# Performance work log

Hardware: AMD Instinct MI355X
Metric: run time of the kernel (lower is better)

Reference implementation:

```python
import jax, jax.numpy as jnp
import numpy as np

N, D_OUT, D_LAT, D_Z = 65536, 128, 64, 64


def setup_inputs() -> dict:
    key = jax.random.key(0)
    ks = jax.random.split(key, 6)
    return {
        "target": jax.random.normal(ks[0], (N, D_OUT), dtype=jnp.float32),
        "output": jax.random.normal(ks[1], (N, D_OUT), dtype=jnp.float32),
        "mean": jax.random.normal(ks[2], (N, D_LAT), dtype=jnp.float32),
        "log_variance": jax.random.normal(ks[3], (N, D_LAT), dtype=jnp.float32),
        "z_t": jax.random.normal(ks[4], (N, D_Z), dtype=jnp.float32),
        "z_t_tau": jax.random.normal(ks[5], (N, D_Z), dtype=jnp.float32),
    }


def reference(target, output, mean, log_variance, z_t, z_t_tau):
    # ELBO: KL(q||N(0,1)) per-sample summed over latent dim, then batch mean
    kl = -0.5 * jnp.sum(log_variance - jnp.exp(log_variance) - mean ** 2 + 1.0, axis=1)
    kl = jnp.mean(kl)
    # reconstruction MSE (weights=None path)
    reconstruction = jnp.mean((output - target) ** 2)
    elbo_loss = reconstruction + kl

    # autocorrelation: diagonal of z_t_centered @ z_t_tau_centered.T is just
    # a rowwise dot product -> O(N*D) instead of O(N^2*D)
    z_t_centered = z_t - jnp.mean(z_t, axis=0)          # [N, D_z]
    z_t_tau_centered = z_t_tau - jnp.mean(z_t_tau, axis=0)
    diag = jnp.sum(z_t_centered * z_t_tau_centered, axis=1)  # [N]
    auto_correlation_loss = -jnp.mean(diag)

    # torch .std() is unbiased (ddof=1)
    std_t = jnp.std(z_t, axis=0, ddof=1)                # [D_z]
    std_tau = jnp.std(z_t_tau, axis=0, ddof=1)
    auto_correlation_loss = auto_correlation_loss / jnp.dot(std_t, std_tau)

    return elbo_loss + auto_correlation_loss
```

## Files before the change

### kernel.cpp

```cpp
#include <hip/hip_runtime.h>

constexpr int N_ROWS  = 65536;
constexpr int THREADS = 256;
constexpr int B_MSE = 1024, B_KL = 512, B_Z = 512;
constexpr int BLOCKS = B_MSE + B_KL + B_Z;
constexpr int F4_BLK = 2048;
constexpr int IT     = F4_BLK / THREADS;

constexpr int NVAL = 324;
constexpr int NREP = 64;

typedef float f4v __attribute__((ext_vector_type(4)));

__device__ __forceinline__ f4v ntload(const f4v* p) {
    return __builtin_nontemporal_load(p);
}


__global__ __launch_bounds__(THREADS) void vde_main(
    const f4v* __restrict__ target,
    const f4v* __restrict__ output,
    const f4v* __restrict__ mean,
    const f4v* __restrict__ logvar,
    const f4v* __restrict__ zt,
    const f4v* __restrict__ ztau,
    float* __restrict__ ws)
{
    const int lane = threadIdx.x & 63;
    const int wave = threadIdx.x >> 6;
    float* rep = ws + (blockIdx.x & (NREP - 1)) * NVAL;

    __shared__ float ssc[4];
    __shared__ float sred[4][16][20];

    if (blockIdx.x < B_MSE) {
        const int base = blockIdx.x * F4_BLK + threadIdx.x;
        float recon = 0.f;
        #pragma unroll
        for (int it = 0; it < IT; ++it) {
            f4v o = ntload(&output[base + it * THREADS]);
            f4v t = ntload(&target[base + it * THREADS]);
            f4v d = o - t;
            recon += d[0]*d[0] + d[1]*d[1] + d[2]*d[2] + d[3]*d[3];
        }
        #pragma unroll
        for (int m = 32; m >= 1; m >>= 1) recon += __shfl_xor(recon, m);
        if (lane == 0) ssc[wave] = recon;
        __syncthreads();
        if (threadIdx.x == 0)
            atomicAdd(&rep[0], ssc[0] + ssc[1] + ssc[2] + ssc[3]);

    } else if (blockIdx.x < B_MSE + B_KL) {
        const int base = (blockIdx.x - B_MSE) * F4_BLK + threadIdx.x;
        float kls = 0.f;
        #pragma unroll
        for (int it = 0; it < IT; ++it) {
            f4v lv = ntload(&logvar[base + it * THREADS]);
            f4v m  = ntload(&mean[base + it * THREADS]);
            kls += (lv[0] - __expf(lv[0]) - m[0]*m[0] + 1.f)
                 + (lv[1] - __expf(lv[1]) - m[1]*m[1] + 1.f)
                 + (lv[2] - __expf(lv[2]) - m[2]*m[2] + 1.f)
                 + (lv[3] - __expf(lv[3]) - m[3]*m[3] + 1.f);
        }
        #pragma unroll
        for (int m = 32; m >= 1; m >>= 1) kls += __shfl_xor(kls, m);
        if (lane == 0) ssc[wave] = kls;
        __syncthreads();
        if (threadIdx.x == 0)
            atomicAdd(&rep[1], ssc[0] + ssc[1] + ssc[2] + ssc[3]);

    } else {
        const int base = (blockIdx.x - B_MSE - B_KL) * F4_BLK + threadIdx.x;
        float s_t[4] = {0,0,0,0}, s_t2[4] = {0,0,0,0};
        float s_a[4] = {0,0,0,0}, s_a2[4] = {0,0,0,0}, s_c[4] = {0,0,0,0};
        #pragma unroll
        for (int it = 0; it < IT; ++it) {
            f4v a = ntload(&zt[base + it * THREADS]);
            f4v b = ntload(&ztau[base + it * THREADS]);
            #pragma unroll
            for (int e = 0; e < 4; ++e) {
                s_t[e]  += a[e];       s_a[e]  += b[e];
                s_t2[e] += a[e]*a[e];  s_a2[e] += b[e]*b[e];
                s_c[e]  += a[e]*b[e];
            }
        }
        float vals[20];
        #pragma unroll
        for (int e = 0; e < 4; ++e) {
            vals[e*5+0] = s_t[e];  vals[e*5+1] = s_a[e];
            vals[e*5+2] = s_t2[e]; vals[e*5+3] = s_a2[e];
            vals[e*5+4] = s_c[e];
        }
        #pragma unroll
        for (int v = 0; v < 20; ++v) {
            vals[v] += __shfl_xor(vals[v], 16);
            vals[v] += __shfl_xor(vals[v], 32);
        }
        if (lane < 16) {
            #pragma unroll
            for (int v = 0; v < 20; ++v) sred[wave][lane][v] = vals[v];
        }
        __syncthreads();
        for (int i = threadIdx.x; i < 320; i += THREADS) {
            const int g = i / 20, v = i % 20;
            const float s = sred[0][g][v] + sred[1][g][v]
                          + sred[2][g][v] + sred[3][g][v];
            const int e = v / 5, st = v % 5;
            atomicAdd(&rep[2 + st * 64 + (g * 4 + e)], s);
        }
    }
}

__global__ __launch_bounds__(256) void vde_tail(
    const float* __restrict__ ws, float* __restrict__ out)
{
    __shared__ float sums[NVAL];
    for (int j = threadIdx.x; j < NVAL; j += 256) {
        float s = 0.f;
        #pragma unroll
        for (int r = 0; r < NREP; ++r) s += ws[r * NVAL + j];
        sums[j] = s;
    }
    __syncthreads();

    if (threadIdx.x < 64) {
        const int j = threadIdx.x;
        const float Nf = (float)N_ROWS;
        const float sum_t  = sums[2 + 0*64 + j];
        const float sum_a  = sums[2 + 1*64 + j];
        const float sum_t2 = sums[2 + 2*64 + j];
        const float sum_a2 = sums[2 + 3*64 + j];
        const float sum_c  = sums[2 + 4*64 + j];

        const float mu_t = sum_t / Nf, mu_a = sum_a / Nf;
        float diag = sum_c - Nf * mu_t * mu_a;
        const float var_t = (sum_t2 - Nf * mu_t * mu_t) / (Nf - 1.f);
        const float var_a = (sum_a2 - Nf * mu_a * mu_a) / (Nf - 1.f);
        float sp = sqrtf(var_t) * sqrtf(var_a);

        #pragma unroll
        for (int m = 32; m >= 1; m >>= 1) {
            diag += __shfl_xor(diag, m);
            sp   += __shfl_xor(sp, m);
        }
        if (j == 0) {
            const float recon_f = sums[0] / (Nf * 128.f);
            const float kl_f    = -0.5f * sums[1] / Nf;
            out[0] = recon_f + kl_f - (diag / Nf) / sp;
        }
    }
}

extern "C" void kernel_launch(void* const* d_in, const int* in_sizes, int n_in,
                              void* d_out, int out_size, void* d_ws, size_t ws_size,
                              hipStream_t stream) {
    const f4v* target = (const f4v*)d_in[0];
    const f4v* output = (const f4v*)d_in[1];
    const f4v* mean   = (const f4v*)d_in[2];
    const f4v* logvar = (const f4v*)d_in[3];
    const f4v* zt     = (const f4v*)d_in[4];
    const f4v* ztau   = (const f4v*)d_in[5];
    float* ws  = (float*)d_ws;
    float* out = (float*)d_out;

    hipMemsetAsync(ws, 0, NREP * NVAL * sizeof(float), stream);
    vde_main<<<BLOCKS, THREADS, 0, stream>>>(target, output, mean, logvar, zt, ztau, ws);
    vde_tail<<<1, 256, 0, stream>>>(ws, out);
}
```

Measured before the change: 148.0 us.

## Fuse tail reduction into main kernel via last-block ticket and per-block partials

Removes the separate tail kernel: each block increments a ticket counter, and the last block to finish does the final reduction and writes the loss. The MSE and KL partials are now plain stores into per-block slots instead of atomics into contended replicas. All loads are issued up front into register arrays to raise memory-level parallelism. This saves one kernel launch and its gap, at the cost of more registers and a serial final reduction inside the last block.

```diff
diff --git a/kernel.cpp b/kernel.cpp
--- a/kernel.cpp
+++ b/kernel.cpp
@@ -7,40 +7,52 @@
 constexpr int F4_BLK = 2048;
 constexpr int IT     = F4_BLK / THREADS;
 
-constexpr int NVAL = 324;
-constexpr int NREP = 64;
+constexpr int NREP  = 64;
+constexpr int NZVAL = 320;
+constexpr int TICKET  = NREP * NZVAL;
+constexpr int MSE_OFF = TICKET + 1;
+constexpr int KL_OFF  = MSE_OFF + B_MSE;
+constexpr int MEMSET_BYTES = (TICKET + 1) * 4;
 
 typedef float f4v __attribute__((ext_vector_type(4)));
 
 __device__ __forceinline__ f4v ntload(const f4v* p) {
     return __builtin_nontemporal_load(p);
 }
-
-
-__global__ __launch_bounds__(THREADS) void vde_main(
+__device__ __forceinline__ float agent_load(const float* p) {
+    return __hip_atomic_load(p, __ATOMIC_RELAXED, __HIP_MEMORY_SCOPE_AGENT);
+}
+__device__ __forceinline__ void agent_store(float* p, float v) {
+    __hip_atomic_store(p, v, __ATOMIC_RELAXED, __HIP_MEMORY_SCOPE_AGENT);
+}
+
+__global__ __launch_bounds__(THREADS) void vde_fused(
     const f4v* __restrict__ target,
     const f4v* __restrict__ output,
     const f4v* __restrict__ mean,
     const f4v* __restrict__ logvar,
     const f4v* __restrict__ zt,
     const f4v* __restrict__ ztau,
-    float* __restrict__ ws)
+    float* __restrict__ ws,
+    float* __restrict__ out)
 {
     const int lane = threadIdx.x & 63;
     const int wave = threadIdx.x >> 6;
-    float* rep = ws + (blockIdx.x & (NREP - 1)) * NVAL;
 
     __shared__ float ssc[4];
     __shared__ float sred[4][16][20];
 
     if (blockIdx.x < B_MSE) {
         const int base = blockIdx.x * F4_BLK + threadIdx.x;
+        f4v o[IT], t[IT];
+        #pragma unroll
+        for (int it = 0; it < IT; ++it) o[it] = ntload(&output[base + it * THREADS]);
+        #pragma unroll
+        for (int it = 0; it < IT; ++it) t[it] = ntload(&target[base + it * THREADS]);
         float recon = 0.f;
         #pragma unroll
         for (int it = 0; it < IT; ++it) {
-            f4v o = ntload(&output[base + it * THREADS]);
-            f4v t = ntload(&target[base + it * THREADS]);
-            f4v d = o - t;
+            f4v d = o[it] - t[it];
             recon += d[0]*d[0] + d[1]*d[1] + d[2]*d[2] + d[3]*d[3];
         }
         #pragma unroll
@@ -48,40 +60,48 @@
         if (lane == 0) ssc[wave] = recon;
         __syncthreads();
         if (threadIdx.x == 0)
-            atomicAdd(&rep[0], ssc[0] + ssc[1] + ssc[2] + ssc[3]);
+            agent_store(&ws[MSE_OFF + blockIdx.x], ssc[0] + ssc[1] + ssc[2] + ssc[3]);
 
     } else if (blockIdx.x < B_MSE + B_KL) {
-        const int base = (blockIdx.x - B_MSE) * F4_BLK + threadIdx.x;
+        const int bi = blockIdx.x - B_MSE;
+        const int base = bi * F4_BLK + threadIdx.x;
+        f4v lv[IT], mm[IT];
+        #pragma unroll
+        for (int it = 0; it < IT; ++it) lv[it] = ntload(&logvar[base + it * THREADS]);
+        #pragma unroll
+        for (int it = 0; it < IT; ++it) mm[it] = ntload(&mean[base + it * THREADS]);
         float kls = 0.f;
         #pragma unroll
         for (int it = 0; it < IT; ++it) {
-            f4v lv = ntload(&logvar[base + it * THREADS]);
-            f4v m  = ntload(&mean[base + it * THREADS]);
-            kls += (lv[0] - __expf(lv[0]) - m[0]*m[0] + 1.f)
-                 + (lv[1] - __expf(lv[1]) - m[1]*m[1] + 1.f)
-                 + (lv[2] - __expf(lv[2]) - m[2]*m[2] + 1.f)
-                 + (lv[3] - __expf(lv[3]) - m[3]*m[3] + 1.f);
+            kls += (lv[it][0] - __expf(lv[it][0]) - mm[it][0]*mm[it][0] + 1.f)
+                 + (lv[it][1] - __expf(lv[it][1]) - mm[it][1]*mm[it][1] + 1.f)
+                 + (lv[it][2] - __expf(lv[it][2]) - mm[it][2]*mm[it][2] + 1.f)
+                 + (lv[it][3] - __expf(lv[it][3]) - mm[it][3]*mm[it][3] + 1.f);
         }
         #pragma unroll
         for (int m = 32; m >= 1; m >>= 1) kls += __shfl_xor(kls, m);
         if (lane == 0) ssc[wave] = kls;
         __syncthreads();
         if (threadIdx.x == 0)
-            atomicAdd(&rep[1], ssc[0] + ssc[1] + ssc[2] + ssc[3]);
+            agent_store(&ws[KL_OFF + bi], ssc[0] + ssc[1] + ssc[2] + ssc[3]);
 
     } else {
-        const int base = (blockIdx.x - B_MSE - B_KL) * F4_BLK + threadIdx.x;
+        const int zi = blockIdx.x - B_MSE - B_KL;
+        const int base = zi * F4_BLK + threadIdx.x;
+        f4v a[IT], b[IT];
+        #pragma unroll
+        for (int it = 0; it < IT; ++it) a[it] = ntload(&zt[base + it * THREADS]);
+        #pragma unroll
+        for (int it = 0; it < IT; ++it) b[it] = ntload(&ztau[base + it * THREADS]);
         float s_t[4] = {0,0,0,0}, s_t2[4] = {0,0,0,0};
         float s_a[4] = {0,0,0,0}, s_a2[4] = {0,0,0,0}, s_c[4] = {0,0,0,0};
         #pragma unroll
         for (int it = 0; it < IT; ++it) {
-            f4v a = ntload(&zt[base + it * THREADS]);
-            f4v b = ntload(&ztau[base + it * THREADS]);
             #pragma unroll
             for (int e = 0; e < 4; ++e) {
-                s_t[e]  += a[e];       s_a[e]  += b[e];
-                s_t2[e] += a[e]*a[e];  s_a2[e] += b[e]*b[e];
-                s_c[e]  += a[e]*b[e];
+                s_t[e]  += a[it][e];          s_a[e]  += b[it][e];
+                s_t2[e] += a[it][e]*a[it][e]; s_a2[e] += b[it][e]*b[it][e];
+                s_c[e]  += a[it][e]*b[it][e];
             }
         }
         float vals[20];
@@ -101,36 +121,54 @@
             for (int v = 0; v < 20; ++v) sred[wave][lane][v] = vals[v];
         }
         __syncthreads();
+        float* rep = ws + (zi & (NREP - 1)) * NZVAL;
         for (int i = threadIdx.x; i < 320; i += THREADS) {
             const int g = i / 20, v = i % 20;
             const float s = sred[0][g][v] + sred[1][g][v]
                           + sred[2][g][v] + sred[3][g][v];
             const int e = v / 5, st = v % 5;
-            atomicAdd(&rep[2 + st * 64 + (g * 4 + e)], s);
-        }
-    }
-}
-
-__global__ __launch_bounds__(256) void vde_tail(
-    const float* __restrict__ ws, float* __restrict__ out)
-{
-    __shared__ float sums[NVAL];
-    for (int j = threadIdx.x; j < NVAL; j += 256) {
+            atomicAdd(&rep[st * 64 + (g * 4 + e)], s);
+        }
+    }
+
+    __shared__ unsigned s_last;
+    __threadfence();
+    if (threadIdx.x == 0) {
+        unsigned* ticket = (unsigned*)&ws[TICKET];
+        s_last = (atomicAdd(ticket, 1u) == (unsigned)(BLOCKS - 1));
+    }
+    __syncthreads();
+    if (!s_last) return;
+    __threadfence();
+
+    __shared__ float zsums[NZVAL];
+    for (int v = threadIdx.x; v < NZVAL; v += THREADS) {
         float s = 0.f;
-        #pragma unroll
-        for (int r = 0; r < NREP; ++r) s += ws[r * NVAL + j];
-        sums[j] = s;
-    }
+        #pragma unroll 8
+        for (int r = 0; r < NREP; ++r) s += agent_load(&ws[r * NZVAL + v]);
+        zsums[v] = s;
+    }
+    float rsum = 0.f;
+    for (int i = threadIdx.x; i < B_MSE; i += THREADS) rsum += agent_load(&ws[MSE_OFF + i]);
+    float ksum = 0.f;
+    for (int i = threadIdx.x; i < B_KL; i += THREADS) ksum += agent_load(&ws[KL_OFF + i]);
+    #pragma unroll
+    for (int m = 32; m >= 1; m >>= 1) {
+        rsum += __shfl_xor(rsum, m);
+        ksum += __shfl_xor(ksum, m);
+    }
+    __shared__ float sc2[4][2];
+    if (lane == 0) { sc2[wave][0] = rsum; sc2[wave][1] = ksum; }
     __syncthreads();
 
     if (threadIdx.x < 64) {
         const int j = threadIdx.x;
         const float Nf = (float)N_ROWS;
-        const float sum_t  = sums[2 + 0*64 + j];
-        const float sum_a  = sums[2 + 1*64 + j];
-        const float sum_t2 = sums[2 + 2*64 + j];
-        const float sum_a2 = sums[2 + 3*64 + j];
-        const float sum_c  = sums[2 + 4*64 + j];
+        const float sum_t  = zsums[0*64 + j];
+        const float sum_a  = zsums[1*64 + j];
+        const float sum_t2 = zsums[2*64 + j];
+        const float sum_a2 = zsums[3*64 + j];
+        const float sum_c  = zsums[4*64 + j];
 
         const float mu_t = sum_t / Nf, mu_a = sum_a / Nf;
         float diag = sum_c - Nf * mu_t * mu_a;
@@ -144,8 +182,8 @@
             sp   += __shfl_xor(sp, m);
         }
         if (j == 0) {
-            const float recon_f = sums[0] / (Nf * 128.f);
-            const float kl_f    = -0.5f * sums[1] / Nf;
+            const float recon_f = (sc2[0][0] + sc2[1][0] + sc2[2][0] + sc2[3][0]) / (Nf * 128.f);
+            const float kl_f    = -0.5f * (sc2[0][1] + sc2[1][1] + sc2[2][1] + sc2[3][1]) / Nf;
             out[0] = recon_f + kl_f - (diag / Nf) / sp;
         }
     }
@@ -163,7 +201,6 @@
     float* ws  = (float*)d_ws;
     float* out = (float*)d_out;
 
-    hipMemsetAsync(ws, 0, NREP * NVAL * sizeof(float), stream);
-    vde_main<<<BLOCKS, THREADS, 0, stream>>>(target, output, mean, logvar, zt, ztau, ws);
-    vde_tail<<<1, 256, 0, stream>>>(ws, out);
-}
+    hipMemsetAsync(ws, 0, MEMSET_BYTES, stream);
+    vde_fused<<<BLOCKS, THREADS, 0, stream>>>(target, output, mean, logvar, zt, ztau, ws, out);
+}
```

Measured after the change: 489.1 us. 3.3x slower.
